# Kernel optimization log

Hardware: AMD Instinct MI355X
Metric: run time of the kernel (lower is better)

The kernel has to match this reference:

```python
import jax, jax.numpy as jnp
import numpy as np


def conv1x1(x, w, b):
    # x: [B,C,H,W], w: [O,C], b: [O]  (1x1 conv == per-pixel matmul)
    return jnp.einsum('oc,bchw->bohw', w, x) + b[None, :, None, None]


def setup_inputs() -> dict:
    key = jax.random.key(0)
    ks = jax.random.split(key, 8)
    B, C, H, W = 8, 256, 64, 64
    heads, points = 8, 4
    x = jax.random.normal(ks[0], (B, C, H, W), dtype=jnp.float32)
    # small offset weights so sampling grids stay mostly in-range (original inits these to 0)
    w_off = jax.random.normal(ks[1], (heads * points * 2, C), dtype=jnp.float32) * 0.01
    b_off = jax.random.normal(ks[2], (heads * points * 2,), dtype=jnp.float32) * 0.05
    w_attn = jax.random.normal(ks[3], (heads * points, C), dtype=jnp.float32) * 0.02
    b_attn = jnp.full((heads * points,), np.log(1.0 / points), dtype=jnp.float32)
    w_val = jax.random.normal(ks[4], (C, C), dtype=jnp.float32) * (1.0 / np.sqrt(C))
    b_val = jnp.zeros((C,), dtype=jnp.float32)
    w_out = jax.random.normal(ks[5], (C, C), dtype=jnp.float32) * (1.0 / np.sqrt(C))
    b_out = jnp.zeros((C,), dtype=jnp.float32)
    return {"x": x, "w_off": w_off, "b_off": b_off, "w_attn": w_attn, "b_attn": b_attn,
            "w_val": w_val, "b_val": b_val, "w_out": w_out, "b_out": b_out,
            "num_heads": heads, "num_points": points}


def _grid_sample_one(v, g):
    # v: [Cph,H,W] value image; g: [P,H,W,2] sampling grid in [-1,1] (x,y), align_corners=True,
    # bilinear, zero padding. Returns [Cph,P,H,W].
    Cph, H, W = v.shape
    ix = (g[..., 0] + 1.0) * 0.5 * (W - 1)  # [P,H,W]
    iy = (g[..., 1] + 1.0) * 0.5 * (H - 1)
    x0 = jnp.floor(ix); y0 = jnp.floor(iy)
    x1 = x0 + 1.0;      y1 = y0 + 1.0
    wx1 = ix - x0; wx0 = 1.0 - wx1
    wy1 = iy - y0; wy0 = 1.0 - wy1

    def corner(yc, xc, w):
        valid = (xc >= 0) & (xc <= W - 1) & (yc >= 0) & (yc <= H - 1)
        yi = jnp.clip(yc, 0, H - 1).astype(jnp.int32)
        xi = jnp.clip(xc, 0, W - 1).astype(jnp.int32)
        vv = v[:, yi, xi]  # [Cph,P,H,W]
        return vv * (w * valid.astype(w.dtype))[None]

    return (corner(y0, x0, wy0 * wx0) + corner(y0, x1, wy0 * wx1)
            + corner(y1, x0, wy1 * wx0) + corner(y1, x1, wy1 * wx1))


def deformable_attention(x, w_off, b_off, w_attn, b_attn, w_val, b_val, w_out, b_out,
                         num_heads, num_points):
    B, C, H, W = x.shape
    hd, P = num_heads, num_points
    cph = C // hd

    value = conv1x1(x, w_val, b_val)                       # [B,C,H,W]
    offsets = conv1x1(x, w_off, b_off)                     # [B,hd*P*2,H,W]
    attn = conv1x1(x, w_attn, b_attn).reshape(B, hd, P, H, W)
    attn = jax.nn.softmax(attn, axis=2)                    # softmax over points

    gy = jnp.linspace(-1.0, 1.0, H, dtype=x.dtype)
    gx = jnp.linspace(-1.0, 1.0, W, dtype=x.dtype)
    base = jnp.stack(jnp.meshgrid(gx, gy, indexing='xy'), axis=-1)  # [H,W,2] (x,y)

    off = offsets.reshape(B, hd, P, 2, H, W).transpose(0, 1, 2, 4, 5, 3)  # [B,hd,P,H,W,2]
    grid = base[None, None, None] + off                                   # [B,hd,P,H,W,2]

    val = value.reshape(B * hd, cph, H, W)
    grid = grid.reshape(B * hd, P, H, W, 2)
    sampled = jax.vmap(_grid_sample_one)(val, grid)        # [B*hd,cph,P,H,W]
    sampled = sampled.reshape(B, hd, cph, P, H, W)

    weighted = (sampled * attn[:, :, None]).sum(axis=3)    # [B,hd,cph,H,W]
    weighted = weighted.reshape(B, C, H, W)
    return conv1x1(weighted, w_out, b_out) + x


def reference(x, w_off, b_off, w_attn, b_attn, w_val, b_val, w_out, b_out,
              num_heads, num_points):
    return deformable_attention(x, w_off, b_off, w_attn, b_attn, w_val, b_val,
                                w_out, b_out, num_heads, num_points)
```

## Files before the change

kernel.cpp:

```cpp
#include <hip/hip_runtime.h>
#include <cstddef>

#define HW 4096
#define WPITCH 256

typedef __attribute__((ext_vector_type(8))) short short8v;
typedef __attribute__((ext_vector_type(4))) float f32x4;

__device__ inline unsigned short f2bf(float f) {
    unsigned int u = __float_as_uint(f);
    u += 0x7FFFu + ((u >> 16) & 1u);
    return (unsigned short)(u >> 16);
}
__device__ inline float bf2f(unsigned short s) {
    return __uint_as_float(((unsigned int)s) << 16);
}

__device__ inline void load_tile2(const unsigned short* __restrict__ g, int kc,
                                  int wid, int lane, short8v r[2])
{
    const int s  = lane & 7;
    const int r8 = lane >> 3;
    const unsigned short* src = g + kc + s * 8;
#pragma unroll
    for (int i = 0; i < 2; ++i) {
        const int row = wid * 16 + i * 8 + r8;
        r[i] = *(const short8v*)(src + row * 256);
    }
}

__device__ inline void store_tile2(unsigned short* lds, int wid, int lane, const short8v r[2])
{
    const int s  = lane & 7;
    const int r8 = lane >> 3;
#pragma unroll
    for (int i = 0; i < 2; ++i) {
        const int row = wid * 16 + i * 8 + r8;
        *(short8v*)((char*)lds + row * 128 + ((s ^ (row & 7)) << 4)) = r[i];
    }
}

__device__ inline short8v read_frag(const unsigned short* lds, int row, int kbyte, int lane)
{
    const char* p = (const char*)lds + row * 128 + (kbyte ^ ((lane & 7) * 16));
    return *(const short8v*)p;
}

__global__ __launch_bounds__(256)
void prep_kernel(const float* __restrict__ w_off, const float* __restrict__ b_off,
                 const float* __restrict__ w_attn, const float* __restrict__ b_attn,
                 const float* __restrict__ w_val, const float* __restrict__ b_val,
                 const float* __restrict__ w_out,
                 unsigned short* __restrict__ wcat_bf, unsigned short* __restrict__ wauxlo,
                 unsigned short* __restrict__ wout_bf, float* __restrict__ bcat)
{
    int i = blockIdx.x * 256 + threadIdx.x;
    if (i < 384 * 256) {
        int n = i >> 8, k = i & 255;
        float v;
        if (n < 256)      v = w_val[n * 256 + k];
        else if (n < 320) v = w_off[(n - 256) * 256 + k];
        else if (n < 352) v = w_attn[(n - 320) * 256 + k];
        else              v = 0.0f;
        unsigned short hi = f2bf(v);
        wcat_bf[i] = hi;
        if (n >= 256) wauxlo[(n - 256) * 256 + k] = f2bf(v - bf2f(hi));
    }
    if (i < 128 * 256) {
        int n = i >> 8;
        if (n >= 96) wauxlo[i] = 0;
    }
    if (i < 256 * 256) wout_bf[i] = f2bf(w_out[i]);
    if (i < 512) {
        float v = 0.0f;
        if (i < 256)      v = b_val[i];
        else if (i < 320) v = b_off[i - 256];
        else if (i < 352) v = b_attn[i - 320];
        bcat[i] = v;
    }
}

__global__ __launch_bounds__(256)
void transpose_kernel(const float* __restrict__ x, unsigned short* __restrict__ xhi)
{
    __shared__ float t[64][65];
    const int bid = blockIdx.x;
    const int pt = bid & 63, ct = (bid >> 6) & 3, b = bid >> 8;
    const int tid = threadIdx.x;
    const int rr = tid >> 4, c4 = (tid & 15) * 4;

    const float* src = x + ((size_t)(b * 256 + ct * 64)) * HW + pt * 64;
#pragma unroll
    for (int j = 0; j < 4; ++j) {
        float4 v = *(const float4*)&src[(size_t)(j * 16 + rr) * HW + c4];
        t[j * 16 + rr][c4 + 0] = v.x; t[j * 16 + rr][c4 + 1] = v.y;
        t[j * 16 + rr][c4 + 2] = v.z; t[j * 16 + rr][c4 + 3] = v.w;
    }
    __syncthreads();

    const size_t obase = ((size_t)b * HW + pt * 64) * 256 + ct * 64;
#pragma unroll
    for (int j = 0; j < 4; ++j) {
        int p = j * 16 + rr;
        ushort4 hi = make_ushort4(f2bf(t[c4 + 0][p]), f2bf(t[c4 + 1][p]),
                                  f2bf(t[c4 + 2][p]), f2bf(t[c4 + 3][p]));
        *(ushort4*)&xhi[obase + (size_t)p * 256 + c4] = hi;
    }
}

__device__ inline void mainloop8(const unsigned short* __restrict__ Ag,
                                 const unsigned short* __restrict__ Bg,
                                 unsigned short* Al, unsigned short* Bl,
                                 int wid, int lane, int wm, int wn, f32x4 acc[4][2])
{
    const int mloc = lane & 15, ksel = lane >> 4;
    short8v rA[2], rB[2];
    load_tile2(Ag, 0, wid, lane, rA);
    load_tile2(Bg, 0, wid, lane, rB);
#pragma unroll
    for (int kc = 0; kc < 4; ++kc) {
        if (kc) __syncthreads();
        store_tile2(Al, wid, lane, rA);
        store_tile2(Bl, wid, lane, rB);
        __syncthreads();
        if (kc < 3) {
            load_tile2(Ag, (kc + 1) * 64, wid, lane, rA);
            load_tile2(Bg, (kc + 1) * 64, wid, lane, rB);
        }
#pragma unroll
        for (int kk = 0; kk < 2; ++kk) {
            const int kb = kk * 64 + ksel * 16;
            short8v a[4], bb[2];
#pragma unroll
            for (int f = 0; f < 4; ++f) a[f]  = read_frag(Al, wm * 64 + f * 16 + mloc, kb, lane);
#pragma unroll
            for (int f = 0; f < 2; ++f) bb[f] = read_frag(Bl, wn * 32 + f * 16 + mloc, kb, lane);
#pragma unroll
            for (int fm = 0; fm < 4; ++fm)
#pragma unroll
                for (int fn = 0; fn < 2; ++fn)
                    acc[fm][fn] = __builtin_amdgcn_mfma_f32_16x16x32_bf16(a[fm], bb[fn], acc[fm][fn], 0, 0, 0);
        }
    }
}

__global__ __launch_bounds__(512)
void proj_kernel(const unsigned short* __restrict__ wcat_bf, const unsigned short* __restrict__ wauxlo,
                 const unsigned short* __restrict__ xhi, const float* __restrict__ bcat,
                 unsigned short* __restrict__ value_bf,
                 float* __restrict__ off_ws, float* __restrict__ attn_ws)
{
    __shared__ unsigned short lds[3 * 128 * 64];
    unsigned short* Al  = lds;
    unsigned short* Bl  = lds + 128 * 64;
    unsigned short* Alo = lds + 2 * 128 * 64;

    const int bid = blockIdx.x;
    const int b    = bid & 7;
    const int rest = bid >> 3;
    const int pt = rest & 31;
    const int mt = rest >> 5;
    const int tid = threadIdx.x, wid = tid >> 6, lane = tid & 63;
    const int wm = wid >> 2, wn = wid & 3;
    const int mloc = lane & 15, ksel = lane >> 4;

    const unsigned short* Bg = xhi + ((size_t)b * HW + pt * 128) * 256;

    f32x4 acc[4][2];
#pragma unroll
    for (int fm = 0; fm < 4; ++fm) {
        float4 bv = *(const float4*)&bcat[mt * 128 + wm * 64 + fm * 16 + ksel * 4];
#pragma unroll
        for (int fn = 0; fn < 2; ++fn) acc[fm][fn] = (f32x4){bv.x, bv.y, bv.z, bv.w};
    }

    if (mt < 2) {
        mainloop8(wcat_bf + mt * 128 * 256, Bg, Al, Bl, wid, lane, wm, wn, acc);

#pragma unroll
        for (int fm = 0; fm < 4; ++fm) {
            const int ch = mt * 128 + wm * 64 + fm * 16 + ksel * 4;
            const int head = ch >> 5, c32 = ch & 31;
#pragma unroll
            for (int fn = 0; fn < 2; ++fn) {
                const int p = pt * 128 + wn * 32 + fn * 16 + mloc;
                f32x4 v = acc[fm][fn];
                ushort4 st = make_ushort4(f2bf(v[0]), f2bf(v[1]), f2bf(v[2]), f2bf(v[3]));
                *(ushort4*)&value_bf[(((size_t)(b * 8 + head)) * HW + p) * 32 + c32] = st;
            }
        }
    } else {
        const unsigned short* Ahg = wcat_bf + 256 * 256;
        const unsigned short* Alg = wauxlo;
        short8v rA[2], rL[2], rB[2];
        load_tile2(Ahg, 0, wid, lane, rA);
        load_tile2(Alg, 0, wid, lane, rL);
        load_tile2(Bg, 0, wid, lane, rB);
#pragma unroll
        for (int kc = 0; kc < 4; ++kc) {
            if (kc) __syncthreads();
            store_tile2(Al, wid, lane, rA);
            store_tile2(Alo, wid, lane, rL);
            store_tile2(Bl, wid, lane, rB);
            __syncthreads();
            if (kc < 3) {
                load_tile2(Ahg, (kc + 1) * 64, wid, lane, rA);
                load_tile2(Alg, (kc + 1) * 64, wid, lane, rL);
                load_tile2(Bg, (kc + 1) * 64, wid, lane, rB);
            }
#pragma unroll
            for (int kk = 0; kk < 2; ++kk) {
                const int kb = kk * 64 + ksel * 16;
                short8v ah[4], al[4], bb[2];
#pragma unroll
                for (int f = 0; f < 4; ++f) {
                    ah[f] = read_frag(Al,  wm * 64 + f * 16 + mloc, kb, lane);
                    al[f] = read_frag(Alo, wm * 64 + f * 16 + mloc, kb, lane);
                }
#pragma unroll
                for (int f = 0; f < 2; ++f) bb[f] = read_frag(Bl, wn * 32 + f * 16 + mloc, kb, lane);
#pragma unroll
                for (int fm = 0; fm < 4; ++fm)
#pragma unroll
                    for (int fn = 0; fn < 2; ++fn) {
                        acc[fm][fn] = __builtin_amdgcn_mfma_f32_16x16x32_bf16(ah[fm], bb[fn], acc[fm][fn], 0, 0, 0);
                        acc[fm][fn] = __builtin_amdgcn_mfma_f32_16x16x32_bf16(al[fm], bb[fn], acc[fm][fn], 0, 0, 0);
                    }
            }
        }
#pragma unroll
        for (int fm = 0; fm < 4; ++fm) {
            const int ch0 = wm * 64 + fm * 16 + ksel * 4;
#pragma unroll
            for (int fn = 0; fn < 2; ++fn) {
                const int p = pt * 128 + wn * 32 + fn * 16 + mloc;
                f32x4 v = acc[fm][fn];
                if (ch0 < 64) {
                    *(float4*)&off_ws[((size_t)b * HW + p) * 64 + ch0] =
                        make_float4(v[0], v[1], v[2], v[3]);
                } else if (ch0 < 96) {
                    float m  = fmaxf(fmaxf(v[0], v[1]), fmaxf(v[2], v[3]));
                    float e0 = __expf(v[0] - m), e1 = __expf(v[1] - m);
                    float e2 = __expf(v[2] - m), e3 = __expf(v[3] - m);
                    float inv = 1.0f / (e0 + e1 + e2 + e3);
                    *(float4*)&attn_ws[((size_t)b * HW + p) * 32 + (ch0 - 64)] =
                        make_float4(e0 * inv, e1 * inv, e2 * inv, e3 * inv);
                }
            }
        }
    }
}

__global__ __launch_bounds__(512, 1)
void sampleout_kernel(const unsigned short* __restrict__ value_bf,
                      const float* __restrict__ off_ws, const float* __restrict__ attn_ws,
                      const unsigned short* __restrict__ wout_bf, const float* __restrict__ b_out,
                      const float* __restrict__ x, float* __restrict__ out)
{
    __shared__ unsigned short Wp[16 * WPITCH];
    __shared__ unsigned short Asm[256 * 64];

    const int bid = blockIdx.x;
    const int b  = bid & 7;
    const int pt = bid >> 3;
    const int tid = threadIdx.x;

    {
        const int c4     = tid & 7;
        const int hh     = (tid >> 3) & 3;
        const int posIdx = tid >> 5;
        const int p      = pt * 16 + posIdx;
        const int h      = p >> 6;
        const int w      = p & 63;
        const float gx = w * (2.0f / 63.0f) - 1.0f;
        const float gy = h * (2.0f / 63.0f) - 1.0f;

        const float* awp  = attn_ws + ((size_t)b * HW + p) * 32;
        const float* offp = off_ws + ((size_t)b * HW + p) * 64;

#pragma unroll
        for (int hq = 0; hq < 2; ++hq) {
            const int head = hh * 2 + hq;
            float4 aw4 = *(const float4*)&awp[head * 4];
            float aw[4] = {aw4.x, aw4.y, aw4.z, aw4.w};
            float4 o01 = *(const float4*)&offp[head * 8];
            float4 o23 = *(const float4*)&offp[head * 8 + 4];
            float oxv[4] = {o01.x, o01.z, o23.x, o23.z};
            float oyv[4] = {o01.y, o01.w, o23.y, o23.w};

            const unsigned short* vb = value_bf + (size_t)(b * 8 + head) * HW * 32 + c4 * 4;

            int   adr[4][4];
            float wc[4][4];
#pragma unroll
            for (int ptq = 0; ptq < 4; ++ptq) {
                float ix = (gx + oxv[ptq] + 1.0f) * 31.5f;
                float iy = (gy + oyv[ptq] + 1.0f) * 31.5f;
                float x0f = floorf(ix), y0f = floorf(iy);
                float wx1 = ix - x0f, wx0 = 1.0f - wx1;
                float wy1 = iy - y0f, wy0 = 1.0f - wy1;
                int x0 = (int)x0f, y0 = (int)y0f;
                int x1 = x0 + 1,   y1 = y0 + 1;
                float a = aw[ptq];
                float vx0 = (x0 >= 0 && x0 <= 63) ? 1.f : 0.f;
                float vx1 = (x1 >= 0 && x1 <= 63) ? 1.f : 0.f;
                float vy0 = (y0 >= 0 && y0 <= 63) ? 1.f : 0.f;
                float vy1 = (y1 >= 0 && y1 <= 63) ? 1.f : 0.f;
                wc[ptq][0] = a * wy0 * wx0 * vy0 * vx0;
                wc[ptq][1] = a * wy0 * wx1 * vy0 * vx1;
                wc[ptq][2] = a * wy1 * wx0 * vy1 * vx0;
                wc[ptq][3] = a * wy1 * wx1 * vy1 * vx1;
                int cx0 = min(max(x0, 0), 63), cx1 = min(max(x1, 0), 63);
                int cy0 = min(max(y0, 0), 63), cy1 = min(max(y1, 0), 63);
                adr[ptq][0] = (cy0 * 64 + cx0) * 32;
                adr[ptq][1] = (cy0 * 64 + cx1) * 32;
                adr[ptq][2] = (cy1 * 64 + cx0) * 32;
                adr[ptq][3] = (cy1 * 64 + cx1) * 32;
            }
            ushort4 u[4][4];
#pragma unroll
            for (int ptq = 0; ptq < 4; ++ptq)
#pragma unroll
                for (int c = 0; c < 4; ++c)
                    u[ptq][c] = *(const ushort4*)&vb[adr[ptq][c]];
            float4 acc = make_float4(0.f, 0.f, 0.f, 0.f);
#pragma unroll
            for (int ptq = 0; ptq < 4; ++ptq)
#pragma unroll
                for (int c = 0; c < 4; ++c) {
                    float wcc = wc[ptq][c];
                    acc.x += wcc * bf2f(u[ptq][c].x);
                    acc.y += wcc * bf2f(u[ptq][c].y);
                    acc.z += wcc * bf2f(u[ptq][c].z);
                    acc.w += wcc * bf2f(u[ptq][c].w);
                }

            const int slot = head * 4 + (c4 >> 1);
            const int byte = posIdx * (WPITCH * 2) + ((slot ^ (posIdx & 7)) << 4) + (c4 & 1) * 8;
            ushort4 st = make_ushort4(f2bf(acc.x), f2bf(acc.y), f2bf(acc.z), f2bf(acc.w));
            *(ushort4*)((char*)Wp + byte) = st;
        }
    }
    __syncthreads();

    const int wid = tid >> 6, lane = tid & 63;
    const int mloc = lane & 15, ksel = lane >> 4;
    const int s = lane & 7, r8 = lane >> 3;

    f32x4 acc2[2];
    acc2[0] = (f32x4){0.f, 0.f, 0.f, 0.f};
    acc2[1] = (f32x4){0.f, 0.f, 0.f, 0.f};

    short8v rA[4];
#pragma unroll
    for (int i = 0; i < 4; ++i)
        rA[i] = *(const short8v*)(wout_bf + (wid * 32 + i * 8 + r8) * 256 + s * 8);

#pragma unroll
    for (int kc = 0; kc < 4; ++kc) {
        if (kc) __syncthreads();
#pragma unroll
        for (int i = 0; i < 4; ++i) {
            const int row = wid * 32 + i * 8 + r8;
            *(short8v*)((char*)Asm + row * 128 + ((s ^ (row & 7)) << 4)) = rA[i];
        }
        __syncthreads();
        if (kc < 3) {
#pragma unroll
            for (int i = 0; i < 4; ++i)
                rA[i] = *(const short8v*)(wout_bf + (wid * 32 + i * 8 + r8) * 256 + (kc + 1) * 64 + s * 8);
        }
#pragma unroll
        for (int kk = 0; kk < 2; ++kk) {
            short8v a[2], bb;
#pragma unroll
            for (int f = 0; f < 2; ++f) {
                const int row = wid * 32 + f * 16 + mloc;
                a[f] = *(const short8v*)((char*)Asm + row * 128 + (((kk * 4 + ksel) ^ (row & 7)) << 4));
            }
            {
                const int row = mloc;
                const int slot = kc * 8 + kk * 4 + ksel;
                bb = *(const short8v*)((char*)Wp + row * (WPITCH * 2) + ((slot ^ (row & 7)) << 4));
            }
#pragma unroll
            for (int fm = 0; fm < 2; ++fm)
                acc2[fm] = __builtin_amdgcn_mfma_f32_16x16x32_bf16(a[fm], bb, acc2[fm], 0, 0, 0);
        }
    }

#pragma unroll
    for (int fm = 0; fm < 2; ++fm) {
        const int o = wid * 32 + fm * 16 + ksel * 4;
        float4 bo = *(const float4*)&b_out[o];
        const int p = pt * 16 + mloc;
        const size_t idx = ((size_t)(b * 256 + o)) * HW + p;
        f32x4 v = acc2[fm];
        out[idx + 0 * HW] = v[0] + bo.x + x[idx + 0 * HW];
        out[idx + 1 * HW] = v[1] + bo.y + x[idx + 1 * HW];
        out[idx + 2 * HW] = v[2] + bo.z + x[idx + 2 * HW];
        out[idx + 3 * HW] = v[3] + bo.w + x[idx + 3 * HW];
    }
}

extern "C" void kernel_launch(void* const* d_in, const int* in_sizes, int n_in,
                              void* d_out, int out_size, void* d_ws, size_t ws_size,
                              hipStream_t stream)
{
    const float* x      = (const float*)d_in[0];
    const float* w_off  = (const float*)d_in[1];
    const float* b_off  = (const float*)d_in[2];
    const float* w_attn = (const float*)d_in[3];
    const float* b_attn = (const float*)d_in[4];
    const float* w_val  = (const float*)d_in[5];
    const float* b_val  = (const float*)d_in[6];
    const float* w_out  = (const float*)d_in[7];
    const float* b_out  = (const float*)d_in[8];
    float* out = (float*)d_out;

    char* ws = (char*)d_ws;
    unsigned short* wcat_bf = (unsigned short*)(ws + 0);
    unsigned short* wauxlo  = (unsigned short*)(ws + 196608);
    unsigned short* wout_bf = (unsigned short*)(ws + 262144);
    float*          bcat    = (float*)(ws + 393216);
    unsigned short* xhi     = (unsigned short*)(ws + 395264);
    unsigned short* val_bf  = (unsigned short*)(ws + 17172480);
    float*          off_ws  = (float*)(ws + 33949696);
    float*          attn_ws = (float*)(ws + 42338304);

    prep_kernel<<<384, 256, 0, stream>>>(w_off, b_off, w_attn, b_attn, w_val, b_val,
                                         w_out, wcat_bf, wauxlo, wout_bf, bcat);
    transpose_kernel<<<2048, 256, 0, stream>>>(x, xhi);
    proj_kernel<<<768, 512, 0, stream>>>(wcat_bf, wauxlo, xhi, bcat, val_bf, off_ws, attn_ws);
    sampleout_kernel<<<2048, 512, 0, stream>>>(val_bf, off_ws, attn_ws, wout_bf, b_out, x, out);
}
```

Baseline: 69.29 us.

## Fuse x transpose/bf16 cast into projection GEMM and widen sampling blocks

Removes the separate transpose kernel and makes the projection GEMM read fp32 x directly in NCHW. Each K-chunk is converted to bf16 and written into the swizzled LDS B tile, which drops a full intermediate write and read of x and one launch. The gathers are strided, though, and the register footprint grows. Separately, the sample+output kernel now uses 1024 threads per block, one head per thread group and one 16-row MFMA fragment per wave, which raises parallelism per block but doubles the threads per block.

```diff
diff --git a/kernel.cpp b/kernel.cpp
--- a/kernel.cpp
+++ b/kernel.cpp
@@ -44,6 +44,30 @@
 {
     const char* p = (const char*)lds + row * 128 + (kbyte ^ ((lane & 7) * 16));
     return *(const short8v*)p;
+}
+
+__device__ inline void load_Bx(const float* __restrict__ Bgx, int kc,
+                               int cg, int pl, float f[16])
+{
+#pragma unroll
+    for (int it = 0; it < 4; ++it) {
+        const int p = pl + it * 32;
+#pragma unroll
+        for (int j = 0; j < 4; ++j)
+            f[it * 4 + j] = Bgx[(size_t)(kc + cg * 4 + j) * HW + p];
+    }
+}
+
+__device__ inline void store_Bx(unsigned short* Bl, int cg, int pl, const float f[16])
+{
+    const int s = cg >> 1, half = cg & 1;
+#pragma unroll
+    for (int it = 0; it < 4; ++it) {
+        const int p = pl + it * 32;
+        ushort4 v = make_ushort4(f2bf(f[it * 4 + 0]), f2bf(f[it * 4 + 1]),
+                                 f2bf(f[it * 4 + 2]), f2bf(f[it * 4 + 3]));
+        *(ushort4*)((char*)Bl + p * 128 + ((s ^ (p & 7)) << 4) + half * 8) = v;
+    }
 }
 
 __global__ __launch_bounds__(256)
@@ -80,73 +104,9 @@
     }
 }
 
-__global__ __launch_bounds__(256)
-void transpose_kernel(const float* __restrict__ x, unsigned short* __restrict__ xhi)
-{
-    __shared__ float t[64][65];
-    const int bid = blockIdx.x;
-    const int pt = bid & 63, ct = (bid >> 6) & 3, b = bid >> 8;
-    const int tid = threadIdx.x;
-    const int rr = tid >> 4, c4 = (tid & 15) * 4;
-
-    const float* src = x + ((size_t)(b * 256 + ct * 64)) * HW + pt * 64;
-#pragma unroll
-    for (int j = 0; j < 4; ++j) {
-        float4 v = *(const float4*)&src[(size_t)(j * 16 + rr) * HW + c4];
-        t[j * 16 + rr][c4 + 0] = v.x; t[j * 16 + rr][c4 + 1] = v.y;
-        t[j * 16 + rr][c4 + 2] = v.z; t[j * 16 + rr][c4 + 3] = v.w;
-    }
-    __syncthreads();
-
-    const size_t obase = ((size_t)b * HW + pt * 64) * 256 + ct * 64;
-#pragma unroll
-    for (int j = 0; j < 4; ++j) {
-        int p = j * 16 + rr;
-        ushort4 hi = make_ushort4(f2bf(t[c4 + 0][p]), f2bf(t[c4 + 1][p]),
-                                  f2bf(t[c4 + 2][p]), f2bf(t[c4 + 3][p]));
-        *(ushort4*)&xhi[obase + (size_t)p * 256 + c4] = hi;
-    }
-}
-
-__device__ inline void mainloop8(const unsigned short* __restrict__ Ag,
-                                 const unsigned short* __restrict__ Bg,
-                                 unsigned short* Al, unsigned short* Bl,
-                                 int wid, int lane, int wm, int wn, f32x4 acc[4][2])
-{
-    const int mloc = lane & 15, ksel = lane >> 4;
-    short8v rA[2], rB[2];
-    load_tile2(Ag, 0, wid, lane, rA);
-    load_tile2(Bg, 0, wid, lane, rB);
-#pragma unroll
-    for (int kc = 0; kc < 4; ++kc) {
-        if (kc) __syncthreads();
-        store_tile2(Al, wid, lane, rA);
-        store_tile2(Bl, wid, lane, rB);
-        __syncthreads();
-        if (kc < 3) {
-            load_tile2(Ag, (kc + 1) * 64, wid, lane, rA);
-            load_tile2(Bg, (kc + 1) * 64, wid, lane, rB);
-        }
-#pragma unroll
-        for (int kk = 0; kk < 2; ++kk) {
-            const int kb = kk * 64 + ksel * 16;
-            short8v a[4], bb[2];
-#pragma unroll
-            for (int f = 0; f < 4; ++f) a[f]  = read_frag(Al, wm * 64 + f * 16 + mloc, kb, lane);
-#pragma unroll
-            for (int f = 0; f < 2; ++f) bb[f] = read_frag(Bl, wn * 32 + f * 16 + mloc, kb, lane);
-#pragma unroll
-            for (int fm = 0; fm < 4; ++fm)
-#pragma unroll
-                for (int fn = 0; fn < 2; ++fn)
-                    acc[fm][fn] = __builtin_amdgcn_mfma_f32_16x16x32_bf16(a[fm], bb[fn], acc[fm][fn], 0, 0, 0);
-        }
-    }
-}
-
 __global__ __launch_bounds__(512)
 void proj_kernel(const unsigned short* __restrict__ wcat_bf, const unsigned short* __restrict__ wauxlo,
-                 const unsigned short* __restrict__ xhi, const float* __restrict__ bcat,
+                 const float* __restrict__ x, const float* __restrict__ bcat,
                  unsigned short* __restrict__ value_bf,
                  float* __restrict__ off_ws, float* __restrict__ attn_ws)
 {
@@ -163,8 +123,9 @@
     const int tid = threadIdx.x, wid = tid >> 6, lane = tid & 63;
     const int wm = wid >> 2, wn = wid & 3;
     const int mloc = lane & 15, ksel = lane >> 4;
-
-    const unsigned short* Bg = xhi + ((size_t)b * HW + pt * 128) * 256;
+    const int cg = tid >> 5, pl = tid & 31;
+
+    const float* Bgx = x + (size_t)b * 256 * HW + pt * 128;
 
     f32x4 acc[4][2];
 #pragma unroll
@@ -175,7 +136,36 @@
     }
 
     if (mt < 2) {
-        mainloop8(wcat_bf + mt * 128 * 256, Bg, Al, Bl, wid, lane, wm, wn, acc);
+        const unsigned short* Ag = wcat_bf + mt * 128 * 256;
+        short8v rA[2];
+        float rBf[16];
+        load_tile2(Ag, 0, wid, lane, rA);
+        load_Bx(Bgx, 0, cg, pl, rBf);
+#pragma unroll
+        for (int kc = 0; kc < 4; ++kc) {
+            if (kc) __syncthreads();
+            store_tile2(Al, wid, lane, rA);
+            store_Bx(Bl, cg, pl, rBf);
+            __syncthreads();
+            if (kc < 3) {
+                load_tile2(Ag, (kc + 1) * 64, wid, lane, rA);
+                load_Bx(Bgx, (kc + 1) * 64, cg, pl, rBf);
+            }
+#pragma unroll
+            for (int kk = 0; kk < 2; ++kk) {
+                const int kb = kk * 64 + ksel * 16;
+                short8v a[4], bb[2];
+#pragma unroll
+                for (int f = 0; f < 4; ++f) a[f]  = read_frag(Al, wm * 64 + f * 16 + mloc, kb, lane);
+#pragma unroll
+                for (int f = 0; f < 2; ++f) bb[f] = read_frag(Bl, wn * 32 + f * 16 + mloc, kb, lane);
+#pragma unroll
+                for (int fm = 0; fm < 4; ++fm)
+#pragma unroll
+                    for (int fn = 0; fn < 2; ++fn)
+                        acc[fm][fn] = __builtin_amdgcn_mfma_f32_16x16x32_bf16(a[fm], bb[fn], acc[fm][fn], 0, 0, 0);
+            }
+        }
 
 #pragma unroll
         for (int fm = 0; fm < 4; ++fm) {
@@ -192,21 +182,22 @@
     } else {
         const unsigned short* Ahg = wcat_bf + 256 * 256;
         const unsigned short* Alg = wauxlo;
-        short8v rA[2], rL[2], rB[2];
+        short8v rA[2], rL[2];
+        float rBf[16];
         load_tile2(Ahg, 0, wid, lane, rA);
         load_tile2(Alg, 0, wid, lane, rL);
-        load_tile2(Bg, 0, wid, lane, rB);
+        load_Bx(Bgx, 0, cg, pl, rBf);
 #pragma unroll
         for (int kc = 0; kc < 4; ++kc) {
             if (kc) __syncthreads();
             store_tile2(Al, wid, lane, rA);
             store_tile2(Alo, wid, lane, rL);
-            store_tile2(Bl, wid, lane, rB);
+            store_Bx(Bl, cg, pl, rBf);
             __syncthreads();
             if (kc < 3) {
                 load_tile2(Ahg, (kc + 1) * 64, wid, lane, rA);
                 load_tile2(Alg, (kc + 1) * 64, wid, lane, rL);
-                load_tile2(Bg, (kc + 1) * 64, wid, lane, rB);
+                load_Bx(Bgx, (kc + 1) * 64, cg, pl, rBf);
             }
 #pragma unroll
             for (int kk = 0; kk < 2; ++kk) {
@@ -251,7 +242,7 @@
     }
 }
 
-__global__ __launch_bounds__(512, 1)
+__global__ __launch_bounds__(1024, 1)
 void sampleout_kernel(const unsigned short* __restrict__ value_bf,
                       const float* __restrict__ off_ws, const float* __restrict__ attn_ws,
                       const unsigned short* __restrict__ wout_bf, const float* __restrict__ b_out,
@@ -267,8 +258,8 @@
 
     {
         const int c4     = tid & 7;
-        const int hh     = (tid >> 3) & 3;
-        const int posIdx = tid >> 5;
+        const int head   = (tid >> 3) & 7;
+        const int posIdx = tid >> 6;
         const int p      = pt * 16 + posIdx;
         const int h      = p >> 6;
         const int w      = p & 63;
@@ -278,128 +269,117 @@
         const float* awp  = attn_ws + ((size_t)b * HW + p) * 32;
         const float* offp = off_ws + ((size_t)b * HW + p) * 64;
 
-#pragma unroll
-        for (int hq = 0; hq < 2; ++hq) {
-            const int head = hh * 2 + hq;
-            float4 aw4 = *(const float4*)&awp[head * 4];
-            float aw[4] = {aw4.x, aw4.y, aw4.z, aw4.w};
-            float4 o01 = *(const float4*)&offp[head * 8];
-            float4 o23 = *(const float4*)&offp[head * 8 + 4];
-            float oxv[4] = {o01.x, o01.z, o23.x, o23.z};
-            float oyv[4] = {o01.y, o01.w, o23.y, o23.w};
-
-            const unsigned short* vb = value_bf + (size_t)(b * 8 + head) * HW * 32 + c4 * 4;
-
-            int   adr[4][4];
-            float wc[4][4];
-#pragma unroll
-            for (int ptq = 0; ptq < 4; ++ptq) {
-                float ix = (gx + oxv[ptq] + 1.0f) * 31.5f;
-                float iy = (gy + oyv[ptq] + 1.0f) * 31.5f;
-                float x0f = floorf(ix), y0f = floorf(iy);
-                float wx1 = ix - x0f, wx0 = 1.0f - wx1;
-                float wy1 = iy - y0f, wy0 = 1.0f - wy1;
-                int x0 = (int)x0f, y0 = (int)y0f;
-                int x1 = x0 + 1,   y1 = y0 + 1;
-                float a = aw[ptq];
-                float vx0 = (x0 >= 0 && x0 <= 63) ? 1.f : 0.f;
-                float vx1 = (x1 >= 0 && x1 <= 63) ? 1.f : 0.f;
-                float vy0 = (y0 >= 0 && y0 <= 63) ? 1.f : 0.f;
-                float vy1 = (y1 >= 0 && y1 <= 63) ? 1.f : 0.f;
-                wc[ptq][0] = a * wy0 * wx0 * vy0 * vx0;
-                wc[ptq][1] = a * wy0 * wx1 * vy0 * vx1;
-                wc[ptq][2] = a * wy1 * wx0 * vy1 * vx0;
-                wc[ptq][3] = a * wy1 * wx1 * vy1 * vx1;
-                int cx0 = min(max(x0, 0), 63), cx1 = min(max(x1, 0), 63);
-                int cy0 = min(max(y0, 0), 63), cy1 = min(max(y1, 0), 63);
-                adr[ptq][0] = (cy0 * 64 + cx0) * 32;
-                adr[ptq][1] = (cy0 * 64 + cx1) * 32;
-                adr[ptq][2] = (cy1 * 64 + cx0) * 32;
-                adr[ptq][3] = (cy1 * 64 + cx1) * 32;
-            }
-            ushort4 u[4][4];
-#pragma unroll
-            for (int ptq = 0; ptq < 4; ++ptq)
-#pragma unroll
-                for (int c = 0; c < 4; ++c)
-                    u[ptq][c] = *(const ushort4*)&vb[adr[ptq][c]];
-            float4 acc = make_float4(0.f, 0.f, 0.f, 0.f);
-#pragma unroll
-            for (int ptq = 0; ptq < 4; ++ptq)
-#pragma unroll
-                for (int c = 0; c < 4; ++c) {
-                    float wcc = wc[ptq][c];
-                    acc.x += wcc * bf2f(u[ptq][c].x);
-                    acc.y += wcc * bf2f(u[ptq][c].y);
-                    acc.z += wcc * bf2f(u[ptq][c].z);
-                    acc.w += wcc * bf2f(u[ptq][c].w);
-                }
-
-            const int slot = head * 4 + (c4 >> 1);
-            const int byte = posIdx * (WPITCH * 2) + ((slot ^ (posIdx & 7)) << 4) + (c4 & 1) * 8;
-            ushort4 st = make_ushort4(f2bf(acc.x), f2bf(acc.y), f2bf(acc.z), f2bf(acc.w));
-            *(ushort4*)((char*)Wp + byte) = st;
-        }
+        float4 aw4 = *(const float4*)&awp[head * 4];
+        float aw[4] = {aw4.x, aw4.y, aw4.z, aw4.w};
+        float4 o01 = *(const float4*)&offp[head * 8];
+        float4 o23 = *(const float4*)&offp[head * 8 + 4];
+        float oxv[4] = {o01.x, o01.z, o23.x, o23.z};
+        float oyv[4] = {o01.y, o01.w, o23.y, o23.w};
+
+        const unsigned short* vb = value_bf + (size_t)(b * 8 + head) * HW * 32 + c4 * 4;
+
+        int   adr[4][4];
+        float wc[4][4];
+#pragma unroll
+        for (int ptq = 0; ptq < 4; ++ptq) {
+            float ix = (gx + oxv[ptq] + 1.0f) * 31.5f;
+            float iy = (gy + oyv[ptq] + 1.0f) * 31.5f;
+            float x0f = floorf(ix), y0f = floorf(iy);
+            float wx1 = ix - x0f, wx0 = 1.0f - wx1;
+            float wy1 = iy - y0f, wy0 = 1.0f - wy1;
+            int x0 = (int)x0f, y0 = (int)y0f;
+            int x1 = x0 + 1,   y1 = y0 + 1;
+            float a = aw[ptq];
+            float vx0 = (x0 >= 0 && x0 <= 63) ? 1.f : 0.f;
+            float vx1 = (x1 >= 0 && x1 <= 63) ? 1.f : 0.f;
+            float vy0 = (y0 >= 0 && y0 <= 63) ? 1.f : 0.f;
+            float vy1 = (y1 >= 0 && y1 <= 63) ? 1.f : 0.f;
+            wc[ptq][0] = a * wy0 * wx0 * vy0 * vx0;
+            wc[ptq][1] = a * wy0 * wx1 * vy0 * vx1;
+            wc[ptq][2] = a * wy1 * wx0 * vy1 * vx0;
+            wc[ptq][3] = a * wy1 * wx1 * vy1 * vx1;
+            int cx0 = min(max(x0, 0), 63), cx1 = min(max(x1, 0), 63);
+            int cy0 = min(max(y0, 0), 63), cy1 = min(max(y1, 0), 63);
+            adr[ptq][0] = (cy0 * 64 + cx0) * 32;
+            adr[ptq][1] = (cy0 * 64 + cx1) * 32;
+            adr[ptq][2] = (cy1 * 64 + cx0) * 32;
+            adr[ptq][3] = (cy1 * 64 + cx1) * 32;
+        }
+        ushort4 u[4][4];
+#pragma unroll
+        for (int ptq = 0; ptq < 4; ++ptq)
+#pragma unroll
+            for (int c = 0; c < 4; ++c)
+                u[ptq][c] = *(const ushort4*)&vb[adr[ptq][c]];
+        float4 acc = make_float4(0.f, 0.f, 0.f, 0.f);
+#pragma unroll
+        for (int ptq = 0; ptq < 4; ++ptq)
+#pragma unroll
+            for (int c = 0; c < 4; ++c) {
+                float wcc = wc[ptq][c];
+                acc.x += wcc * bf2f(u[ptq][c].x);
+                acc.y += wcc * bf2f(u[ptq][c].y);
+                acc.z += wcc * bf2f(u[ptq][c].z);
+                acc.w += wcc * bf2f(u[ptq][c].w);
+            }
+
+        const int slot = head * 4 + (c4 >> 1);
+        const int byte = posIdx * (WPITCH * 2) + ((slot ^ (posIdx & 7)) << 4) + (c4 & 1) * 8;
+        ushort4 st = make_ushort4(f2bf(acc.x), f2bf(acc.y), f2bf(acc.z), f2bf(acc.w));
+        *(ushort4*)((char*)Wp + byte) = st;
     }
     __syncthreads();
 
     const int wid = tid >> 6, lane = tid & 63;
     const int mloc = lane & 15, ksel = lane >> 4;
-    const int s = lane & 7, r8 = lane >> 3;
-
-    f32x4 acc2[2];
-    acc2[0] = (f32x4){0.f, 0.f, 0.f, 0.f};
-    acc2[1] = (f32x4){0.f, 0.f, 0.f, 0.f};
-
-    short8v rA[4];
-#pragma unroll
-    for (int i = 0; i < 4; ++i)
-        rA[i] = *(const short8v*)(wout_bf + (wid * 32 + i * 8 + r8) * 256 + s * 8);
+    const int sA = tid & 7, rr = tid >> 3;
+
+    f32x4 acc2 = (f32x4){0.f, 0.f, 0.f, 0.f};
+
+    short8v rA[2];
+#pragma unroll
+    for (int i = 0; i < 2; ++i)
+        rA[i] = *(const short8v*)(wout_bf + (rr + i * 128) * 256 + sA * 8);
 
 #pragma unroll
     for (int kc = 0; kc < 4; ++kc) {
         if (kc) __syncthreads();
 #pragma unroll
-        for (int i = 0; i < 4; ++i) {
-            const int row = wid * 32 + i * 8 + r8;
-            *(short8v*)((char*)Asm + row * 128 + ((s ^ (row & 7)) << 4)) = rA[i];
+        for (int i = 0; i < 2; ++i) {
+            const int row = rr + i * 128;
+            *(short8v*)((char*)Asm + row * 128 + ((sA ^ (row & 7)) << 4)) = rA[i];
         }
         __syncthreads();
         if (kc < 3) {
 #pragma unroll
-            for (int i = 0; i < 4; ++i)
-                rA[i] = *(const short8v*)(wout_bf + (wid * 32 + i * 8 + r8) * 256 + (kc + 1) * 64 + s * 8);
+            for (int i = 0; i < 2; ++i)
+                rA[i] = *(const short8v*)(wout_bf + (rr + i * 128) * 256 + (kc + 1) * 64 + sA * 8);
         }
 #pragma unroll
         for (int kk = 0; kk < 2; ++kk) {
-            short8v a[2], bb;
-#pragma unroll
-            for (int f = 0; f < 2; ++f) {
-                const int row = wid * 32 + f * 16 + mloc;
-                a[f] = *(const short8v*)((char*)Asm + row * 128 + (((kk * 4 + ksel) ^ (row & 7)) << 4));
+            short8v a, bb;
+            {
+                const int row = wid * 16 + mloc;
+                a = *(const short8v*)((char*)Asm + row * 128 + (((kk * 4 + ksel) ^ (row & 7)) << 4));
             }
             {
                 const int row = mloc;
                 const int slot = kc * 8 + kk * 4 + ksel;
                 bb = *(const short8v*)((char*)Wp + row * (WPITCH * 2) + ((slot ^ (row & 7)) << 4));
             }
-#pragma unroll
-            for (int fm = 0; fm < 2; ++fm)
-                acc2[fm] = __builtin_amdgcn_mfma_f32_16x16x32_bf16(a[fm], bb, acc2[fm], 0, 0, 0);
-        }
-    }
-
-#pragma unroll
-    for (int fm = 0; fm < 2; ++fm) {
-        const int o = wid * 32 + fm * 16 + ksel * 4;
+            acc2 = __builtin_amdgcn_mfma_f32_16x16x32_bf16(a, bb, acc2, 0, 0, 0);
+        }
+    }
+
+    {
+        const int o = wid * 16 + ksel * 4;
         float4 bo = *(const float4*)&b_out[o];
         const int p = pt * 16 + mloc;
         const size_t idx = ((size_t)(b * 256 + o)) * HW + p;
-        f32x4 v = acc2[fm];
-        out[idx + 0 * HW] = v[0] + bo.x + x[idx + 0 * HW];
-        out[idx + 1 * HW] = v[1] + bo.y + x[idx + 1 * HW];
-        out[idx + 2 * HW] = v[2] + bo.z + x[idx + 2 * HW];
-        out[idx + 3 * HW] = v[3] + bo.w + x[idx + 3 * HW];
+        out[idx + 0 * HW] = acc2[0] + bo.x + x[idx + 0 * HW];
+        out[idx + 1 * HW] = acc2[1] + bo.y + x[idx + 1 * HW];
+        out[idx + 2 * HW] = acc2[2] + bo.z + x[idx + 2 * HW];
+        out[idx + 3 * HW] = acc2[3] + bo.w + x[idx + 3 * HW];
     }
 }
 
@@ -423,14 +403,12 @@
     unsigned short* wauxlo  = (unsigned short*)(ws + 196608);
     unsigned short* wout_bf = (unsigned short*)(ws + 262144);
     float*          bcat    = (float*)(ws + 393216);
-    unsigned short* xhi     = (unsigned short*)(ws + 395264);
-    unsigned short* val_bf  = (unsigned short*)(ws + 17172480);
-    float*          off_ws  = (float*)(ws + 33949696);
-    float*          attn_ws = (float*)(ws + 42338304);
+    unsigned short* val_bf  = (unsigned short*)(ws + 395264);
+    float*          off_ws  = (float*)(ws + 17172480);
+    float*          attn_ws = (float*)(ws + 25561088);
 
     prep_kernel<<<384, 256, 0, stream>>>(w_off, b_off, w_attn, b_attn, w_val, b_val,
                                          w_out, wcat_bf, wauxlo, wout_bf, bcat);
-    transpose_kernel<<<2048, 256, 0, stream>>>(x, xhi);
-    proj_kernel<<<768, 512, 0, stream>>>(wcat_bf, wauxlo, xhi, bcat, val_bf, off_ws, attn_ws);
-    sampleout_kernel<<<2048, 512, 0, stream>>>(val_bf, off_ws, attn_ws, wout_bf, b_out, x, out);
-}
+    proj_kernel<<<768, 512, 0, stream>>>(wcat_bf, wauxlo, x, bcat, val_bf, off_ws, attn_ws);
+    sampleout_kernel<<<2048, 1024, 0, stream>>>(val_bf, off_ws, attn_ws, wout_bf, b_out, x, out);
+}
```

Result: slower. 82.98 us (+19.8%).
